# Kernel tuning notes

Hardware: AMD Instinct MI355X
Metric: run time of the kernel (lower is better)

## Reference

```python
import jax, jax.numpy as jnp
import numpy as np

EPS = 1e-8  # PoissonNLLLoss default eps

def _pair_loss(inp, tgt):
    # Poisson NLL (log_input=False, full=True), summed over detector dim D,
    # for every (hypothesis i, measurement j) pair WITHOUT materializing [N,M,D]:
    # loss_ij = sum_d inp[i,d] - sum_d tgt[j,d]*log(inp[i,d]+eps) + sum_d stirling(tgt[j,d])
    log_in = jnp.log(inp + EPS)                         # [N,D]
    s_in = jnp.sum(inp, axis=1)                         # [N]
    cross = jnp.einsum('id,jd->ij', log_in, tgt)        # [N,M]
    t_safe = jnp.where(tgt > 1, tgt, 1.0)
    stirling = jnp.where(
        tgt > 1,
        tgt * jnp.log(t_safe) - tgt + 0.5 * jnp.log(2.0 * jnp.pi * t_safe),
        0.0,
    )
    s_st = jnp.sum(stirling, axis=1)                    # [M]
    return s_in[:, None] - cross + s_st[None, :]        # [N,M]

def setup_inputs() -> dict:
    key = jax.random.key(0)
    k1, k2 = jax.random.split(key)
    N, M, D = 10000, 10000, 180
    # photon-count-like positive values; scale so target>1 hits Stirling branch
    inp = jax.random.uniform(k1, (N, D), dtype=jnp.float32) * 100.0
    tgt = jax.random.uniform(k2, (M, D), dtype=jnp.float32) * 100.0
    return {"input": inp, "target": tgt}

def reference(input, target):
    L = _pair_loss(input, target)          # [N,M]
    loss_v = jnp.min(L, axis=1)            # [N]
    match = jnp.argmin(L, axis=1)          # [N] int
    loss = jnp.mean(loss_v)
    return (loss, match)
```

## Files before the change

### kernel.cpp

```cpp
#include <hip/hip_runtime.h>
#include <math.h>

#define EPSF 1e-8f

typedef _Float16 f16x8 __attribute__((ext_vector_type(8)));
typedef float f32x4 __attribute__((ext_vector_type(4)));

#define GLOAD_LDS16(g, l)                                                      \
  __builtin_amdgcn_global_load_lds(                                            \
      (const __attribute__((address_space(1))) unsigned int*)(g),              \
      (__attribute__((address_space(3))) unsigned int*)(l), 16, 0, 0)

#define WAITV(n) asm volatile("s_waitcnt vmcnt(" #n ")" ::: "memory")
#define BAR() __builtin_amdgcn_s_barrier()

__device__ __forceinline__ unsigned int ord_from_float(float f) {
  unsigned int u = __float_as_uint(f);
  return (u & 0x80000000u) ? ~u : (u | 0x80000000u);
}

__device__ __forceinline__ float float_from_ord(unsigned int o) {
  return (o & 0x80000000u) ? __uint_as_float(o & 0x7fffffffu)
                           : __uint_as_float(~o);
}

__device__ __forceinline__ unsigned long long shfl_xor_u64(unsigned long long x, int m) {
  int lo = __shfl_xor((int)(unsigned int)(x & 0xffffffffull), m, 64);
  int hi = __shfl_xor((int)(unsigned int)(x >> 32), m, 64);
  return ((unsigned long long)(unsigned int)hi << 32) | (unsigned int)lo;
}

__global__ __launch_bounds__(64) void prep_A_kernel(
    const float* __restrict__ inp, _Float16* __restrict__ Acat,
    float* __restrict__ s_in, unsigned long long* __restrict__ packed,
    int N, int D, int DP, int KPA) {
  int r = blockIdx.x;
  _Float16* row = Acat + (size_t)r * KPA;
  float s = 0.f;
  for (int d = threadIdx.x; d < DP; d += 64) {
    float lg = 0.f;
    if (r < N && d < D) {
      float x = inp[(size_t)r * D + d];
      s += x;
      lg = logf(x + EPSF);
    }
    _Float16 h = (_Float16)lg;
    _Float16 l = (_Float16)(lg - (float)h);
    row[d] = h;
    row[DP + d] = h;
    row[2 * DP + d] = l;
  }
  for (int d = threadIdx.x; d < KPA - 3 * DP; d += 64) row[3 * DP + d] = (_Float16)0.f;
  #pragma unroll
  for (int m = 1; m < 64; m <<= 1) s += __shfl_xor(s, m, 64);
  if (threadIdx.x == 0 && r < N) {
    s_in[r] = s;
    packed[r] = ~0ull;
  }
}

__global__ __launch_bounds__(64) void prep_B_kernel(
    const float* __restrict__ tgt, _Float16* __restrict__ Bcat,
    float* __restrict__ s_st, int M, int D, int DP, int KPA) {
  int r = blockIdx.x;
  _Float16* row = Bcat + (size_t)r * KPA;
  float s = 0.f;
  for (int d = threadIdx.x; d < DP; d += 64) {
    float x = 0.f;
    if (r < M && d < D) {
      x = tgt[(size_t)r * D + d];
      if (x > 1.0f)
        s += x * logf(x) - x + 0.5f * logf(6.283185307179586f * x);
    }
    _Float16 h = (_Float16)x;
    _Float16 l = (_Float16)(x - (float)h);
    row[d] = h;
    row[DP + d] = l;
    row[2 * DP + d] = h;
  }
  for (int d = threadIdx.x; d < KPA - 3 * DP; d += 64) row[3 * DP + d] = (_Float16)0.f;
  #pragma unroll
  for (int m = 1; m < 64; m <<= 1) s += __shfl_xor(s, m, 64);
  if (threadIdx.x == 0 && r < M) s_st[r] = s;
}

#define BT 256
#define UNITH 8192

__global__ __launch_bounds__(512, 2) void mfma_pair_min_kernel(
    const _Float16* __restrict__ Acat, const _Float16* __restrict__ Bcat,
    const float* __restrict__ s_st, unsigned long long* __restrict__ packed,
    int N, int M, int KPA, int gx) {
  extern __shared__ __align__(16) _Float16 smem[];
  const int t = threadIdx.x;
  const int lane = t & 63;
  const int wid = t >> 6;
  const int wr = wid >> 2;
  const int wc = wid & 3;

  const int nwg = gridDim.x;
  const int q8 = nwg >> 3;
  const int xcd = blockIdx.x & 7;
  const int i8 = blockIdx.x >> 3;
  int brow, bcol;
  if (q8 % gx == 0) {
    int bh = q8 / gx;
    brow = xcd * bh + i8 % bh;
    bcol = i8 / bh;
  } else {
    int wg = xcd * q8 + i8;
    brow = wg / gx;
    bcol = wg % gx;
  }
  const int row0 = brow * BT;
  const int col0 = bcol * BT;

  f32x4 acc[8][4] = {};

  const int srow = lane >> 2;
  const int gs = (lane & 3) ^ ((lane >> 3) & 3);
  const _Float16* a0 = Acat + (size_t)(row0 + wid * 32 + srow) * KPA + gs * 8;
  const _Float16* a1 = a0 + (size_t)16 * KPA;
  const _Float16* b0 = Bcat + (size_t)(col0 + wid * 32 + srow) * KPA + gs * 8;
  const _Float16* b1 = b0 + (size_t)16 * KPA;

#define STAGE(buf_)                                                            \
  do {                                                                         \
    _Float16* dA_ = smem + (buf_) * 2 * UNITH + wid * 1024;                    \
    _Float16* dB_ = dA_ + UNITH;                                               \
    GLOAD_LDS16(a0, dA_);                                                      \
    GLOAD_LDS16(a1, dA_ + 512);                                                \
    GLOAD_LDS16(b0, dB_);                                                      \
    GLOAD_LDS16(b1, dB_ + 512);                                                \
  } while (0)

#define ADV() do { a0 += 32; a1 += 32; b0 += 32; b1 += 32; } while (0)

  const int rl = lane & 15;
  const int qq = lane >> 4;
  const int sa = qq ^ ((rl >> 1) & 3);

#define COMPUTE(buf_)                                                          \
  do {                                                                         \
    const _Float16* pA_ = smem + (buf_) * 2 * UNITH;                           \
    const _Float16* pB_ = pA_ + UNITH;                                         \
    f16x8 af[8], bf[4];                                                        \
    _Pragma("unroll")                                                          \
    for (int m = 0; m < 8; ++m)                                                \
      af[m] = *(const f16x8*)(pA_ + (wr * 128 + m * 16 + rl) * 32 + sa * 8);   \
    _Pragma("unroll")                                                          \
    for (int n = 0; n < 4; ++n)                                                \
      bf[n] = *(const f16x8*)(pB_ + (wc * 64 + n * 16 + rl) * 32 + sa * 8);    \
    __builtin_amdgcn_s_setprio(1);                                             \
    _Pragma("unroll")                                                          \
    for (int m = 0; m < 8; ++m)                                                \
      _Pragma("unroll")                                                        \
      for (int n = 0; n < 4; ++n)                                              \
        acc[m][n] = __builtin_amdgcn_mfma_f32_16x16x32_f16(af[m], bf[n],       \
                                                           acc[m][n], 0, 0, 0); \
    __builtin_amdgcn_s_setprio(0);                                             \
  } while (0)

  const int NT = KPA >> 5;

  STAGE(0);
  WAITV(0);
  BAR();
  for (int kt = 0; kt < NT - 1; ++kt) {
    ADV();
    STAGE((kt + 1) & 1);
    COMPUTE(kt & 1);
    WAITV(0);
    BAR();
  }
  COMPUTE((NT - 1) & 1);

#undef STAGE
#undef ADV
#undef COMPUTE

  float stv[4];
  #pragma unroll
  for (int n = 0; n < 4; ++n) {
    int gj = col0 + wc * 64 + n * 16 + rl;
    stv[n] = (gj < M) ? s_st[gj] : __builtin_inff();
  }
  #pragma unroll
  for (int m = 0; m < 8; ++m) {
    #pragma unroll
    for (int g = 0; g < 4; ++g) {
      int grow = row0 + wr * 128 + m * 16 + qq * 4 + g;
      unsigned long long bst = ~0ull;
      #pragma unroll
      for (int n = 0; n < 4; ++n) {
        int gj = col0 + wc * 64 + n * 16 + rl;
        float val = stv[n] - acc[m][n][g];
        unsigned long long p =
            ((unsigned long long)ord_from_float(val) << 32) | (unsigned int)gj;
        if (p < bst) bst = p;
      }
      #pragma unroll
      for (int mm = 1; mm < 16; mm <<= 1) {
        unsigned long long o = shfl_xor_u64(bst, mm);
        if (o < bst) bst = o;
      }
      if (rl == 0 && grow < N) atomicMin(&packed[grow], bst);
    }
  }
}


__global__ __launch_bounds__(256) void finalize_kernel(
    const unsigned long long* __restrict__ packed,
    const float* __restrict__ s_in, float* __restrict__ out, int N) {
  __shared__ double sh[256];
  double s = 0.0;
  for (int i = threadIdx.x; i < N; i += 256) {
    unsigned long long p = packed[i];
    float val = float_from_ord((unsigned int)(p >> 32));
    out[1 + i] = (float)(unsigned int)(p & 0xffffffffull);
    s += (double)(s_in[i] + val);
  }
  sh[threadIdx.x] = s;
  __syncthreads();
  for (int off = 128; off > 0; off >>= 1) {
    if (threadIdx.x < off) sh[threadIdx.x] += sh[threadIdx.x + off];
    __syncthreads();
  }
  if (threadIdx.x == 0) out[0] = (float)(sh[0] / N);
}

extern "C" void kernel_launch(void* const* d_in, const int* in_sizes, int n_in,
                              void* d_out, int out_size, void* d_ws, size_t ws_size,
                              hipStream_t stream) {
  const float* inp = (const float*)d_in[0];
  const float* tgt = (const float*)d_in[1];
  float* out = (float*)d_out;

  int N = out_size - 1;
  int D = in_sizes[0] / N;
  int M = in_sizes[1] / D;

  int Npad = ((N + BT - 1) / BT) * BT;
  int Mpad = ((M + BT - 1) / BT) * BT;
  int DP = ((D + 31) / 32) * 32;
  int KPA = ((3 * DP + 31) / 32) * 32;

  char* ws = (char*)d_ws;
  size_t off = 0;
  float* s_in = (float*)(ws + off); off += (size_t)N * 4;
  float* s_st = (float*)(ws + off); off += (size_t)M * 4;
  off = (off + 15) & ~(size_t)15;
  unsigned long long* packed = (unsigned long long*)(ws + off); off += (size_t)N * 8;
  off = (off + 15) & ~(size_t)15;
  _Float16* Acat = (_Float16*)(ws + off); off += (size_t)Npad * KPA * 2;
  _Float16* Bcat = (_Float16*)(ws + off); off += (size_t)Mpad * KPA * 2;

  prep_A_kernel<<<Npad, 64, 0, stream>>>(inp, Acat, s_in, packed, N, D, DP, KPA);
  prep_B_kernel<<<Mpad, 64, 0, stream>>>(tgt, Bcat, s_st, M, D, DP, KPA);

  const int ldsBytes = 4 * UNITH * 2;
  hipFuncSetAttribute((const void*)mfma_pair_min_kernel,
                      hipFuncAttributeMaxDynamicSharedMemorySize, ldsBytes);

  int gx = Mpad / BT, gy = Npad / BT;
  mfma_pair_min_kernel<<<gx * gy, 512, ldsBytes, stream>>>(Acat, Bcat, s_st,
                                                           packed, N, M, KPA, gx);

  finalize_kernel<<<1, 256, 0, stream>>>(packed, s_in, out, N);
}
```

Measured before the change: 208.4 us.

## Shrink GEMM tile to 128, fuse prep kernels, parallelize final reduction

The two prep kernels become one launch. The pair GEMM tile shrinks from 256x256 with 512 threads to 128x128 with 256 threads, using static LDS and a column-major XCD-aware block mapping. The single-block finalize is split into a multi-block reduce that accumulates a fixed-point sum with integer atomics, followed by a tiny final kernel. The smaller tile gives more blocks, which helps occupancy and load balance, but it halves operand reuse and doubles the atomicMin traffic on the packed row minima.

After: 267.5 us. +28.4%, slower.

```diff
diff --git a/kernel.cpp b/kernel.cpp
--- a/kernel.cpp
+++ b/kernel.cpp
@@ -30,92 +30,87 @@
   return ((unsigned long long)(unsigned int)hi << 32) | (unsigned int)lo;
 }
 
-__global__ __launch_bounds__(64) void prep_A_kernel(
-    const float* __restrict__ inp, _Float16* __restrict__ Acat,
-    float* __restrict__ s_in, unsigned long long* __restrict__ packed,
-    int N, int D, int DP, int KPA) {
-  int r = blockIdx.x;
-  _Float16* row = Acat + (size_t)r * KPA;
-  float s = 0.f;
-  for (int d = threadIdx.x; d < DP; d += 64) {
-    float lg = 0.f;
-    if (r < N && d < D) {
-      float x = inp[(size_t)r * D + d];
-      s += x;
-      lg = logf(x + EPSF);
-    }
-    _Float16 h = (_Float16)lg;
-    _Float16 l = (_Float16)(lg - (float)h);
-    row[d] = h;
-    row[DP + d] = h;
-    row[2 * DP + d] = l;
-  }
-  for (int d = threadIdx.x; d < KPA - 3 * DP; d += 64) row[3 * DP + d] = (_Float16)0.f;
-  #pragma unroll
-  for (int m = 1; m < 64; m <<= 1) s += __shfl_xor(s, m, 64);
-  if (threadIdx.x == 0 && r < N) {
-    s_in[r] = s;
-    packed[r] = ~0ull;
-  }
-}
-
-__global__ __launch_bounds__(64) void prep_B_kernel(
-    const float* __restrict__ tgt, _Float16* __restrict__ Bcat,
-    float* __restrict__ s_st, int M, int D, int DP, int KPA) {
-  int r = blockIdx.x;
-  _Float16* row = Bcat + (size_t)r * KPA;
-  float s = 0.f;
-  for (int d = threadIdx.x; d < DP; d += 64) {
-    float x = 0.f;
-    if (r < M && d < D) {
-      x = tgt[(size_t)r * D + d];
-      if (x > 1.0f)
-        s += x * logf(x) - x + 0.5f * logf(6.283185307179586f * x);
-    }
-    _Float16 h = (_Float16)x;
-    _Float16 l = (_Float16)(x - (float)h);
-    row[d] = h;
-    row[DP + d] = l;
-    row[2 * DP + d] = h;
-  }
-  for (int d = threadIdx.x; d < KPA - 3 * DP; d += 64) row[3 * DP + d] = (_Float16)0.f;
-  #pragma unroll
-  for (int m = 1; m < 64; m <<= 1) s += __shfl_xor(s, m, 64);
-  if (threadIdx.x == 0 && r < M) s_st[r] = s;
-}
-
-#define BT 256
-#define UNITH 8192
-
-__global__ __launch_bounds__(512, 2) void mfma_pair_min_kernel(
+__global__ __launch_bounds__(64) void prep_kernel(
+    const float* __restrict__ inp, const float* __restrict__ tgt,
+    _Float16* __restrict__ Acat, _Float16* __restrict__ Bcat,
+    float* __restrict__ s_in, float* __restrict__ s_st,
+    unsigned long long* __restrict__ packed,
+    int N, int M, int Npad, int Mpad, int D, int DP, int KPA) {
+  const int r = blockIdx.x;
+  if (r < Npad) {
+    _Float16* row = Acat + (size_t)r * KPA;
+    float s = 0.f;
+    for (int d = threadIdx.x; d < DP; d += 64) {
+      float lg = 0.f;
+      if (r < N && d < D) {
+        float x = inp[(size_t)r * D + d];
+        s += x;
+        lg = logf(x + EPSF);
+      }
+      _Float16 h = (_Float16)lg;
+      _Float16 l = (_Float16)(lg - (float)h);
+      row[d] = h;
+      row[DP + d] = h;
+      row[2 * DP + d] = l;
+    }
+    for (int d = threadIdx.x; d < KPA - 3 * DP; d += 64)
+      row[3 * DP + d] = (_Float16)0.f;
+    #pragma unroll
+    for (int m = 1; m < 64; m <<= 1) s += __shfl_xor(s, m, 64);
+    if (threadIdx.x == 0 && r < N) {
+      s_in[r] = s;
+      packed[r] = ~0ull;
+    }
+  }
+  if (r < Mpad) {
+    _Float16* row = Bcat + (size_t)r * KPA;
+    float s = 0.f;
+    for (int d = threadIdx.x; d < DP; d += 64) {
+      float x = 0.f;
+      if (r < M && d < D) {
+        x = tgt[(size_t)r * D + d];
+        if (x > 1.0f)
+          s += x * logf(x) - x + 0.5f * logf(6.283185307179586f * x);
+      }
+      _Float16 h = (_Float16)x;
+      _Float16 l = (_Float16)(x - (float)h);
+      row[d] = h;
+      row[DP + d] = l;
+      row[2 * DP + d] = h;
+    }
+    for (int d = threadIdx.x; d < KPA - 3 * DP; d += 64)
+      row[3 * DP + d] = (_Float16)0.f;
+    #pragma unroll
+    for (int m = 1; m < 64; m <<= 1) s += __shfl_xor(s, m, 64);
+    if (threadIdx.x == 0 && r < M) s_st[r] = s;
+  }
+}
+
+#define BT 128
+
+__global__ __launch_bounds__(256) void mfma_pair_min_kernel(
     const _Float16* __restrict__ Acat, const _Float16* __restrict__ Bcat,
     const float* __restrict__ s_st, unsigned long long* __restrict__ packed,
-    int N, int M, int KPA, int gx) {
-  extern __shared__ __align__(16) _Float16 smem[];
+    int N, int M, int KPA, int gy) {
+  __shared__ __align__(16) _Float16 Ash[2][BT * 32];
+  __shared__ __align__(16) _Float16 Bsh[2][BT * 32];
   const int t = threadIdx.x;
   const int lane = t & 63;
   const int wid = t >> 6;
-  const int wr = wid >> 2;
-  const int wc = wid & 3;
+  const int wr = wid >> 1;
+  const int wc = wid & 1;
 
   const int nwg = gridDim.x;
-  const int q8 = nwg >> 3;
+  const int q = nwg >> 3, r8 = nwg & 7;
   const int xcd = blockIdx.x & 7;
-  const int i8 = blockIdx.x >> 3;
-  int brow, bcol;
-  if (q8 % gx == 0) {
-    int bh = q8 / gx;
-    brow = xcd * bh + i8 % bh;
-    bcol = i8 / bh;
-  } else {
-    int wg = xcd * q8 + i8;
-    brow = wg / gx;
-    bcol = wg % gx;
-  }
+  const int idx = blockIdx.x >> 3;
+  const int wg = (xcd < r8 ? xcd * (q + 1) : r8 * (q + 1) + (xcd - r8) * q) + idx;
+  const int brow = wg % gy;
+  const int bcol = wg / gy;
   const int row0 = brow * BT;
   const int col0 = bcol * BT;
 
-  f32x4 acc[8][4] = {};
+  f32x4 acc[4][4] = {};
 
   const int srow = lane >> 2;
   const int gs = (lane & 3) ^ ((lane >> 3) & 3);
@@ -126,12 +121,10 @@
 
 #define STAGE(buf_)                                                            \
   do {                                                                         \
-    _Float16* dA_ = smem + (buf_) * 2 * UNITH + wid * 1024;                    \
-    _Float16* dB_ = dA_ + UNITH;                                               \
-    GLOAD_LDS16(a0, dA_);                                                      \
-    GLOAD_LDS16(a1, dA_ + 512);                                                \
-    GLOAD_LDS16(b0, dB_);                                                      \
-    GLOAD_LDS16(b1, dB_ + 512);                                                \
+    GLOAD_LDS16(a0, &Ash[buf_][wid * 1024]);                                   \
+    GLOAD_LDS16(a1, &Ash[buf_][wid * 1024 + 512]);                             \
+    GLOAD_LDS16(b0, &Bsh[buf_][wid * 1024]);                                   \
+    GLOAD_LDS16(b1, &Bsh[buf_][wid * 1024 + 512]);                             \
   } while (0)
 
 #define ADV() do { a0 += 32; a1 += 32; b0 += 32; b1 += 32; } while (0)
@@ -142,18 +135,16 @@
 
 #define COMPUTE(buf_)                                                          \
   do {                                                                         \
-    const _Float16* pA_ = smem + (buf_) * 2 * UNITH;                           \
-    const _Float16* pB_ = pA_ + UNITH;                                         \
-    f16x8 af[8], bf[4];                                                        \
+    f16x8 af[4], bf[4];                                                        \
     _Pragma("unroll")                                                          \
-    for (int m = 0; m < 8; ++m)                                                \
-      af[m] = *(const f16x8*)(pA_ + (wr * 128 + m * 16 + rl) * 32 + sa * 8);   \
+    for (int m = 0; m < 4; ++m)                                                \
+      af[m] = *(const f16x8*)(&Ash[buf_][(wr * 64 + m * 16 + rl) * 32 + sa * 8]); \
     _Pragma("unroll")                                                          \
     for (int n = 0; n < 4; ++n)                                                \
-      bf[n] = *(const f16x8*)(pB_ + (wc * 64 + n * 16 + rl) * 32 + sa * 8);    \
+      bf[n] = *(const f16x8*)(&Bsh[buf_][(wc * 64 + n * 16 + rl) * 32 + sa * 8]); \
     __builtin_amdgcn_s_setprio(1);                                             \
     _Pragma("unroll")                                                          \
-    for (int m = 0; m < 8; ++m)                                                \
+    for (int m = 0; m < 4; ++m)                                                \
       _Pragma("unroll")                                                        \
       for (int n = 0; n < 4; ++n)                                              \
         acc[m][n] = __builtin_amdgcn_mfma_f32_16x16x32_f16(af[m], bf[n],       \
@@ -186,10 +177,10 @@
     stv[n] = (gj < M) ? s_st[gj] : __builtin_inff();
   }
   #pragma unroll
-  for (int m = 0; m < 8; ++m) {
+  for (int m = 0; m < 4; ++m) {
     #pragma unroll
     for (int g = 0; g < 4; ++g) {
-      int grow = row0 + wr * 128 + m * 16 + qq * 4 + g;
+      int grow = row0 + wr * 64 + m * 16 + qq * 4 + g;
       unsigned long long bst = ~0ull;
       #pragma unroll
       for (int n = 0; n < 4; ++n) {
@@ -209,25 +200,35 @@
   }
 }
 
-
-__global__ __launch_bounds__(256) void finalize_kernel(
+__global__ __launch_bounds__(256) void reduce_kernel(
     const unsigned long long* __restrict__ packed,
-    const float* __restrict__ s_in, float* __restrict__ out, int N) {
+    const float* __restrict__ s_in, float* __restrict__ out,
+    unsigned long long* __restrict__ sumbuf, int N) {
+  int i = blockIdx.x * 256 + threadIdx.x;
+  double local = 0.0;
+  if (i < N) {
+    unsigned long long p = packed[i];
+    out[1 + i] = (float)(unsigned int)(p & 0xffffffffull);
+    float val = float_from_ord((unsigned int)(p >> 32));
+    local = (double)(s_in[i] + val);
+  }
   __shared__ double sh[256];
-  double s = 0.0;
-  for (int i = threadIdx.x; i < N; i += 256) {
-    unsigned long long p = packed[i];
-    float val = float_from_ord((unsigned int)(p >> 32));
-    out[1 + i] = (float)(unsigned int)(p & 0xffffffffull);
-    s += (double)(s_in[i] + val);
-  }
-  sh[threadIdx.x] = s;
+  sh[threadIdx.x] = local;
   __syncthreads();
-  for (int off = 128; off > 0; off >>= 1) {
-    if (threadIdx.x < off) sh[threadIdx.x] += sh[threadIdx.x + off];
+  for (int o = 128; o > 0; o >>= 1) {
+    if (threadIdx.x < o) sh[threadIdx.x] += sh[threadIdx.x + o];
     __syncthreads();
   }
-  if (threadIdx.x == 0) out[0] = (float)(sh[0] / N);
+  if (threadIdx.x == 0) {
+    long long qv = __double2ll_rn(sh[0] * 1048576.0);
+    atomicAdd(sumbuf, (unsigned long long)qv);
+  }
+}
+
+__global__ void final_kernel(const unsigned long long* __restrict__ sumbuf,
+                             float* __restrict__ out, int N) {
+  if (threadIdx.x == 0)
+    out[0] = (float)(((double)(long long)sumbuf[0] / 1048576.0) / (double)N);
 }
 
 extern "C" void kernel_launch(void* const* d_in, const int* in_sizes, int n_in,
@@ -245,27 +246,29 @@
   int Mpad = ((M + BT - 1) / BT) * BT;
   int DP = ((D + 31) / 32) * 32;
   int KPA = ((3 * DP + 31) / 32) * 32;
+  int gx = Mpad / BT, gy = Npad / BT;
 
   char* ws = (char*)d_ws;
   size_t off = 0;
   float* s_in = (float*)(ws + off); off += (size_t)N * 4;
   float* s_st = (float*)(ws + off); off += (size_t)M * 4;
   off = (off + 15) & ~(size_t)15;
+  unsigned long long* sumbuf = (unsigned long long*)(ws + off); off += 16;
   unsigned long long* packed = (unsigned long long*)(ws + off); off += (size_t)N * 8;
   off = (off + 15) & ~(size_t)15;
   _Float16* Acat = (_Float16*)(ws + off); off += (size_t)Npad * KPA * 2;
   _Float16* Bcat = (_Float16*)(ws + off); off += (size_t)Mpad * KPA * 2;
 
-  prep_A_kernel<<<Npad, 64, 0, stream>>>(inp, Acat, s_in, packed, N, D, DP, KPA);
-  prep_B_kernel<<<Mpad, 64, 0, stream>>>(tgt, Bcat, s_st, M, D, DP, KPA);
-
-  const int ldsBytes = 4 * UNITH * 2;
-  hipFuncSetAttribute((const void*)mfma_pair_min_kernel,
-                      hipFuncAttributeMaxDynamicSharedMemorySize, ldsBytes);
-
-  int gx = Mpad / BT, gy = Npad / BT;
-  mfma_pair_min_kernel<<<gx * gy, 512, ldsBytes, stream>>>(Acat, Bcat, s_st,
-                                                           packed, N, M, KPA, gx);
-
-  finalize_kernel<<<1, 256, 0, stream>>>(packed, s_in, out, N);
-}
+  hipMemsetAsync(sumbuf, 0, 8, stream);
+
+  int pgrid = Npad > Mpad ? Npad : Mpad;
+  prep_kernel<<<pgrid, 64, 0, stream>>>(inp, tgt, Acat, Bcat, s_in, s_st,
+                                        packed, N, M, Npad, Mpad, D, DP, KPA);
+
+  mfma_pair_min_kernel<<<gx * gy, 256, 0, stream>>>(Acat, Bcat, s_st, packed,
+                                                    N, M, KPA, gy);
+
+  reduce_kernel<<<(N + 255) / 256, 256, 0, stream>>>(packed, s_in, out,
+                                                     sumbuf, N);
+  final_kernel<<<1, 64, 0, stream>>>(sumbuf, out, N);
+}
```
